# Kernel optimization log

Measured on AMD Instinct MI355X. Metric: run time of the kernel, lower is better.

The kernel has to match this reference:

```python
import jax, jax.numpy as jnp
import numpy as np

B, S, H = 64, 2048, 256


def setup_inputs() -> dict:
    key = jax.random.key(0)
    k1, k2, k3, k4 = jax.random.split(key, 4)
    text = jax.random.normal(k1, (B, S, H), dtype=jnp.float32)
    aspect = jax.random.normal(k2, (B, S, H), dtype=jnp.float32)
    r = 0.01  # uniform_rate from reset_parameters
    W_text = jax.random.uniform(k3, (H, H), dtype=jnp.float32, minval=-r, maxval=r)
    W_combine = jax.random.uniform(k4, (1, 2 * H), dtype=jnp.float32, minval=-r, maxval=r)
    return {"text": text, "aspect": aspect, "W_text": W_text, "W_combine": W_combine}


def reference(text, aspect, W_text, W_combine):
    # NOTE: original module applies w_text to BOTH text and aspect (w_aspect unused).
    m_text = jnp.einsum("bsh,kh->bsk", text, W_text)      # [B,S,H]
    m_aspect = jnp.einsum("bsh,kh->bsk", aspect, W_text)  # [B,S,H]
    combine = jnp.tanh(jnp.concatenate([m_text, m_aspect], axis=2))  # [B,S,2H]
    score = jnp.einsum("bsk,ok->bso", combine, W_combine)  # [B,S,1]
    weight = jax.nn.softmax(score, axis=1)                  # softmax over seq dim
    weight = jnp.transpose(weight, (0, 2, 1))               # [B,1,S]
    out = jnp.matmul(weight, text)                          # [B,1,H]
    return (weight, out)
```

## Files before the change

### kernel.cpp

```cpp
#include <hip/hip_runtime.h>
#include <hip/hip_bf16.h>

#define BB 64
#define SS 2048
#define HH 256

typedef __attribute__((ext_vector_type(8))) __bf16 bf16x8;
typedef __attribute__((ext_vector_type(4))) float f32x4;

typedef __attribute__((address_space(1))) const unsigned int g_u32;
typedef __attribute__((address_space(3))) unsigned int l_u32;

__device__ __forceinline__ float tanh_fast(float x) {
  float e = __expf(2.0f * x);
  return __fdividef(e - 1.0f, e + 1.0f);
}

__global__ __launch_bounds__(1024) void cvt_w_kernel(const float* __restrict__ w,
                                                     __bf16* __restrict__ wb) {
  int i = blockIdx.x * 1024 + threadIdx.x;
  wb[i] = (__bf16)w[i];
}

__global__ __launch_bounds__(256, 2) void score_kernel(
    const float* __restrict__ text, const float* __restrict__ aspect,
    const __bf16* __restrict__ wbf, const float* __restrict__ wc,
    float* __restrict__ scores_t, float* __restrict__ scores_a) {
  __shared__ float smem[4 * 16 * 256 + 256];
  float* partial = smem + 4 * 16 * 256;

  const int tid = threadIdx.x;
  const int lane = tid & 63;
  const int wid = tid >> 6;
  const int fr = lane & 15;
  const int fq = lane >> 4;

  const float* tbase = (wid & 2) ? aspect : text;
  const long r0 = (long)blockIdx.x * 32 + ((wid & 1) << 4);
#pragma unroll
  for (int it = 0; it < 16; ++it) {
    const int sig = ((it & 7) << 3) | (it >> 3);
    const char* g = (const char*)(tbase + (r0 + it) * HH) + ((lane ^ sig) << 4);
    float* l = smem + wid * 4096 + it * 256;
    __builtin_amdgcn_global_load_lds((g_u32*)g, (l_u32*)l, 16, 0, 0);
  }
  __syncthreads();

  bf16x8 afr[4][8];
  const int sig_fr = ((fr & 7) << 3) | (fr >> 3);
#pragma unroll
  for (int set = 0; set < 4; ++set) {
    const char* base = (const char*)(smem + set * 4096 + fr * 256);
#pragma unroll
    for (int c = 0; c < 8; ++c) {
      const int u0 = c * 8 + fq * 2;
      f32x4 v0 = *(const f32x4*)(base + ((u0 ^ sig_fr) << 4));
      f32x4 v1 = *(const f32x4*)(base + (((u0 + 1) ^ sig_fr) << 4));
      bf16x8 t;
#pragma unroll
      for (int j = 0; j < 4; ++j) {
        t[j] = (__bf16)v0[j];
        t[4 + j] = (__bf16)v1[j];
      }
      afr[set][c] = t;
    }
  }

  float sp[4][4];
#pragma unroll
  for (int a = 0; a < 4; ++a)
#pragma unroll
    for (int j = 0; j < 4; ++j) sp[a][j] = 0.f;

#pragma unroll 1
  for (int i = 0; i < 4; ++i) {
    const int nt = wid * 4 + i;
    const __bf16* wp = wbf + (nt * 16 + fr) * HH + fq * 8;
    bf16x8 bfr[8];
#pragma unroll
    for (int c = 0; c < 8; ++c) bfr[c] = *(const bf16x8*)(wp + c * 32);
    const float wct = wc[nt * 16 + fr];
    const float wca = wc[HH + nt * 16 + fr];
#pragma unroll
    for (int set = 0; set < 4; ++set) {
      f32x4 cacc = {0.f, 0.f, 0.f, 0.f};
#pragma unroll
      for (int c = 0; c < 8; ++c)
        cacc = __builtin_amdgcn_mfma_f32_16x16x32_bf16(afr[set][c], bfr[c], cacc, 0, 0, 0);
      const float wcv = (set & 2) ? wca : wct;
#pragma unroll
      for (int j = 0; j < 4; ++j) sp[set][j] += tanh_fast(cacc[j]) * wcv;
    }
  }

#pragma unroll
  for (int off = 1; off < 16; off <<= 1)
#pragma unroll
    for (int set = 0; set < 4; ++set)
#pragma unroll
      for (int j = 0; j < 4; ++j) sp[set][j] += __shfl_xor(sp[set][j], off, 64);
  if (fr == 0) {
#pragma unroll
    for (int set = 0; set < 4; ++set)
#pragma unroll
      for (int j = 0; j < 4; ++j)
        partial[wid * 64 + set * 16 + fq * 4 + j] = sp[set][j];
  }
  __syncthreads();
  if (tid < 64) {
    float s = partial[tid] + partial[64 + tid] + partial[128 + tid] + partial[192 + tid];
    float* dst = (tid & 32) ? scores_a : scores_t;
    dst[(long)blockIdx.x * 32 + (tid & 31)] = s;
  }
}

__global__ __launch_bounds__(256) void softmax_kernel(
    const float* __restrict__ st, const float* __restrict__ sa,
    float* __restrict__ weight, float* __restrict__ out2) {
  const int b = blockIdx.x;
  const int tid = threadIdx.x;
  const int lane = tid & 63;
  const int wid = tid >> 6;
  float v[8];
  float mx = -1e30f;
#pragma unroll
  for (int i = 0; i < 8; ++i) {
    const long idx = (long)b * SS + tid + i * 256;
    v[i] = st[idx] + sa[idx];
    mx = fmaxf(mx, v[i]);
  }
#pragma unroll
  for (int off = 32; off >= 1; off >>= 1) mx = fmaxf(mx, __shfl_xor(mx, off, 64));
  __shared__ float red[8];
  if (lane == 0) red[wid] = mx;
  __syncthreads();
  mx = fmaxf(fmaxf(red[0], red[1]), fmaxf(red[2], red[3]));
  float sum = 0.f;
#pragma unroll
  for (int i = 0; i < 8; ++i) {
    v[i] = __expf(v[i] - mx);
    sum += v[i];
  }
#pragma unroll
  for (int off = 32; off >= 1; off >>= 1) sum += __shfl_xor(sum, off, 64);
  if (lane == 0) red[4 + wid] = sum;
  __syncthreads();
  sum = red[4] + red[5] + red[6] + red[7];
  const float inv = 1.0f / sum;
#pragma unroll
  for (int i = 0; i < 8; ++i) weight[(long)b * SS + tid + i * 256] = v[i] * inv;
  out2[b * HH + tid] = 0.0f;
}

__global__ __launch_bounds__(256) void out_kernel(const float* __restrict__ text,
                                                  const float* __restrict__ weight,
                                                  float* __restrict__ out2) {
  const int b = blockIdx.x >> 5;
  const int ch = blockIdx.x & 31;
  const int tid = threadIdx.x;
  __shared__ float wsm[64];
  if (tid < 64) wsm[tid] = weight[(long)b * SS + ch * 64 + tid];
  __syncthreads();
  const float* t = text + ((long)b * SS + ch * 64) * HH;
  float acc = 0.f;
#pragma unroll 8
  for (int s = 0; s < 64; ++s) acc = fmaf(wsm[s], t[(long)s * HH + tid], acc);
  atomicAdd(&out2[b * HH + tid], acc);
}

extern "C" void kernel_launch(void* const* d_in, const int* in_sizes, int n_in,
                              void* d_out, int out_size, void* d_ws, size_t ws_size,
                              hipStream_t stream) {
  const float* text = (const float*)d_in[0];
  const float* aspect = (const float*)d_in[1];
  const float* w = (const float*)d_in[2];
  const float* wc = (const float*)d_in[3];

  float* weight = (float*)d_out;
  float* out2 = weight + (long)BB * SS;

  float* scores_t = (float*)d_ws;
  float* scores_a = scores_t + (long)BB * SS;
  __bf16* wbf = (__bf16*)(scores_a + (long)BB * SS);

  cvt_w_kernel<<<dim3(64), dim3(1024), 0, stream>>>(w, wbf);
  score_kernel<<<dim3(4096), dim3(256), 0, stream>>>(text, aspect, wbf, wc,
                                                     scores_t, scores_a);
  softmax_kernel<<<dim3(BB), dim3(256), 0, stream>>>(scores_t, scores_a, weight, out2);
  out_kernel<<<dim3(BB * 32), dim3(256), 0, stream>>>(text, weight, out2);
}
```

Measured before the change: 345.0 us.

## Make score kernel persistent with register-staged double-buffered bf16 LDS tiles

```diff
diff --git a/kernel.cpp b/kernel.cpp
--- a/kernel.cpp
+++ b/kernel.cpp
@@ -4,16 +4,22 @@
 #define BB 64
 #define SS 2048
 #define HH 256
+#define NTILES 16
+#define TROWS 32
 
 typedef __attribute__((ext_vector_type(8))) __bf16 bf16x8;
 typedef __attribute__((ext_vector_type(4))) float f32x4;
-
-typedef __attribute__((address_space(1))) const unsigned int g_u32;
-typedef __attribute__((address_space(3))) unsigned int l_u32;
 
 __device__ __forceinline__ float tanh_fast(float x) {
   float e = __expf(2.0f * x);
   return __fdividef(e - 1.0f, e + 1.0f);
+}
+
+__device__ __forceinline__ bf16x8 pack8(f32x4 a, f32x4 b) {
+  bf16x8 r;
+  r[0] = (__bf16)a[0]; r[1] = (__bf16)a[1]; r[2] = (__bf16)a[2]; r[3] = (__bf16)a[3];
+  r[4] = (__bf16)b[0]; r[5] = (__bf16)b[1]; r[6] = (__bf16)b[2]; r[7] = (__bf16)b[3];
+  return r;
 }
 
 __global__ __launch_bounds__(1024) void cvt_w_kernel(const float* __restrict__ w,
@@ -22,96 +28,110 @@
   wb[i] = (__bf16)w[i];
 }
 
-__global__ __launch_bounds__(256, 2) void score_kernel(
+__global__ __launch_bounds__(512, 2) void score_kernel(
     const float* __restrict__ text, const float* __restrict__ aspect,
     const __bf16* __restrict__ wbf, const float* __restrict__ wc,
     float* __restrict__ scores_t, float* __restrict__ scores_a) {
-  __shared__ float smem[4 * 16 * 256 + 256];
-  float* partial = smem + 4 * 16 * 256;
+  __shared__ __bf16 sbuf[2][64][256];
+  __shared__ float pr[2][8][2][2][16];
 
   const int tid = threadIdx.x;
   const int lane = tid & 63;
   const int wid = tid >> 6;
   const int fr = lane & 15;
   const int fq = lane >> 4;
-
-  const float* tbase = (wid & 2) ? aspect : text;
-  const long r0 = (long)blockIdx.x * 32 + ((wid & 1) << 4);
-#pragma unroll
-  for (int it = 0; it < 16; ++it) {
-    const int sig = ((it & 7) << 3) | (it >> 3);
-    const char* g = (const char*)(tbase + (r0 + it) * HH) + ((lane ^ sig) << 4);
-    float* l = smem + wid * 4096 + it * 256;
-    __builtin_amdgcn_global_load_lds((g_u32*)g, (l_u32*)l, 16, 0, 0);
-  }
-  __syncthreads();
-
-  bf16x8 afr[4][8];
-  const int sig_fr = ((fr & 7) << 3) | (fr >> 3);
-#pragma unroll
-  for (int set = 0; set < 4; ++set) {
-    const char* base = (const char*)(smem + set * 4096 + fr * 256);
-#pragma unroll
-    for (int c = 0; c < 8; ++c) {
-      const int u0 = c * 8 + fq * 2;
-      f32x4 v0 = *(const f32x4*)(base + ((u0 ^ sig_fr) << 4));
-      f32x4 v1 = *(const f32x4*)(base + (((u0 + 1) ^ sig_fr) << 4));
-      bf16x8 t;
-#pragma unroll
-      for (int j = 0; j < 4; ++j) {
-        t[j] = (__bf16)v0[j];
-        t[4 + j] = (__bf16)v1[j];
+  const long blockRow0 = (long)blockIdx.x * (NTILES * TROWS);
+
+  bf16x8 wf[2][8];
+  float wcv[2][2][4];
+#pragma unroll
+  for (int nti = 0; nti < 2; ++nti) {
+    const int nt = wid * 2 + nti;
+    const __bf16* wp = wbf + (nt * 16 + fr) * HH + fq * 8;
+#pragma unroll
+    for (int c = 0; c < 8; ++c) wf[nti][c] = *(const bf16x8*)(wp + c * 32);
+#pragma unroll
+    for (int r = 0; r < 4; ++r) {
+      wcv[0][nti][r] = wc[nt * 16 + fq * 4 + r];
+      wcv[1][nti][r] = wc[HH + nt * 16 + fq * 4 + r];
+    }
+  }
+
+  f32x4 reg[8];
+
+  auto issue_loads = [&](int t) {
+    const long R = blockRow0 + (long)t * TROWS;
+#pragma unroll
+    for (int rr = 0; rr < 4; ++rr) {
+      const int cr = wid * 8 + rr * 2 + (lane >> 5);
+      const float* base = (cr & 32) ? aspect : text;
+      const float* p = base + (R + (cr & 31)) * HH + (lane & 31) * 8;
+      reg[rr * 2] = *(const f32x4*)p;
+      reg[rr * 2 + 1] = *(const f32x4*)(p + 4);
+    }
+  };
+  auto write_stage = [&](int pb) {
+#pragma unroll
+    for (int rr = 0; rr < 4; ++rr) {
+      const int cr = wid * 8 + rr * 2 + (lane >> 5);
+      const int up = (lane & 31) ^ (cr & 7);
+      *(bf16x8*)&sbuf[pb][cr][up * 8] = pack8(reg[rr * 2], reg[rr * 2 + 1]);
+    }
+  };
+  auto compute = [&](int pb, int par) {
+#pragma unroll
+    for (int set = 0; set < 2; ++set)
+#pragma unroll
+      for (int half = 0; half < 2; ++half) {
+        const int cr = set * 32 + half * 16 + fr;
+        const __bf16* rowp = &sbuf[pb][cr][0];
+        bf16x8 tf[8];
+#pragma unroll
+        for (int c = 0; c < 8; ++c) {
+          const int u = c * 4 + fq;
+          tf[c] = *(const bf16x8*)(rowp + (u ^ (fr & 7)) * 8);
+        }
+        f32x4 a0 = {0.f, 0.f, 0.f, 0.f}, a1 = {0.f, 0.f, 0.f, 0.f};
+#pragma unroll
+        for (int c = 0; c < 8; ++c) {
+          a0 = __builtin_amdgcn_mfma_f32_16x16x32_bf16(wf[0][c], tf[c], a0, 0, 0, 0);
+          a1 = __builtin_amdgcn_mfma_f32_16x16x32_bf16(wf[1][c], tf[c], a1, 0, 0, 0);
+        }
+        float p = 0.f;
+#pragma unroll
+        for (int r = 0; r < 4; ++r)
+          p += tanh_fast(a0[r]) * wcv[set][0][r] + tanh_fast(a1[r]) * wcv[set][1][r];
+        p += __shfl_xor(p, 16, 64);
+        p += __shfl_xor(p, 32, 64);
+        if (fq == 0) pr[par][wid][set][half][fr] = p;
       }
-      afr[set][c] = t;
-    }
-  }
-
-  float sp[4][4];
-#pragma unroll
-  for (int a = 0; a < 4; ++a)
-#pragma unroll
-    for (int j = 0; j < 4; ++j) sp[a][j] = 0.f;
+  };
+  auto reduce_out = [&](int t) {
+    if (tid < 64) {
+      const int par = t & 1;
+      const int set = tid >> 5;
+      const int r = tid & 31;
+      float s = 0.f;
+#pragma unroll
+      for (int w = 0; w < 8; ++w) s += pr[par][w][set][r >> 4][r & 15];
+      (set ? scores_a : scores_t)[blockRow0 + (long)t * TROWS + r] = s;
+    }
+  };
+
+  issue_loads(0);
+  write_stage(0);
+  __syncthreads();
 
 #pragma unroll 1
-  for (int i = 0; i < 4; ++i) {
-    const int nt = wid * 4 + i;
-    const __bf16* wp = wbf + (nt * 16 + fr) * HH + fq * 8;
-    bf16x8 bfr[8];
-#pragma unroll
-    for (int c = 0; c < 8; ++c) bfr[c] = *(const bf16x8*)(wp + c * 32);
-    const float wct = wc[nt * 16 + fr];
-    const float wca = wc[HH + nt * 16 + fr];
-#pragma unroll
-    for (int set = 0; set < 4; ++set) {
-      f32x4 cacc = {0.f, 0.f, 0.f, 0.f};
-#pragma unroll
-      for (int c = 0; c < 8; ++c)
-        cacc = __builtin_amdgcn_mfma_f32_16x16x32_bf16(afr[set][c], bfr[c], cacc, 0, 0, 0);
-      const float wcv = (set & 2) ? wca : wct;
-#pragma unroll
-      for (int j = 0; j < 4; ++j) sp[set][j] += tanh_fast(cacc[j]) * wcv;
-    }
-  }
-
-#pragma unroll
-  for (int off = 1; off < 16; off <<= 1)
-#pragma unroll
-    for (int set = 0; set < 4; ++set)
-#pragma unroll
-      for (int j = 0; j < 4; ++j) sp[set][j] += __shfl_xor(sp[set][j], off, 64);
-  if (fr == 0) {
-#pragma unroll
-    for (int set = 0; set < 4; ++set)
-#pragma unroll
-      for (int j = 0; j < 4; ++j)
-        partial[wid * 64 + set * 16 + fq * 4 + j] = sp[set][j];
-  }
-  __syncthreads();
-  if (tid < 64) {
-    float s = partial[tid] + partial[64 + tid] + partial[128 + tid] + partial[192 + tid];
-    float* dst = (tid & 32) ? scores_a : scores_t;
-    dst[(long)blockIdx.x * 32 + (tid & 31)] = s;
-  }
+  for (int t = 0; t < NTILES; ++t) {
+    const int pb = t & 1;
+    if (t + 1 < NTILES) issue_loads(t + 1);
+    if (t > 0) reduce_out(t - 1);
+    compute(pb, t & 1);
+    if (t + 1 < NTILES) write_stage(pb ^ 1);
+    __syncthreads();
+  }
+  reduce_out(NTILES - 1);
 }
 
 __global__ __launch_bounds__(256) void softmax_kernel(
@@ -184,8 +204,8 @@
   __bf16* wbf = (__bf16*)(scores_a + (long)BB * SS);
 
   cvt_w_kernel<<<dim3(64), dim3(1024), 0, stream>>>(w, wbf);
-  score_kernel<<<dim3(4096), dim3(256), 0, stream>>>(text, aspect, wbf, wc,
-                                                     scores_t, scores_a);
+  score_kernel<<<dim3(256), dim3(512), 0, stream>>>(text, aspect, wbf, wc,
+                                                    scores_t, scores_a);
   softmax_kernel<<<dim3(BB), dim3(256), 0, stream>>>(scores_t, scores_a, weight, out2);
   out_kernel<<<dim3(BB * 32), dim3(256), 0, stream>>>(text, weight, out2);
 }
```

Measured after the change: 317.8 us. 1.09x faster.
